# Performance work log

Measured on AMD Instinct MI355X. Metric: run time of the kernel, lower is better.

## Reference

```python
import jax, jax.numpy as jnp
import numpy as np

N, D, K = 262144, 64, 1024


def setup_inputs() -> dict:
    key = jax.random.key(0)
    kx, kc = jax.random.split(key)
    x = jax.random.normal(kx, (N, D), dtype=jnp.float32)
    codebook = jax.random.normal(kc, (K, D), dtype=jnp.float32)
    return {"x": x, "codebook": codebook}


def reference(x, codebook):
    # VQTokenizer.encode: cdist(x, codebook) -> argmin -> gather.
    # squared distances equals argmin over cdist (sqrt is monotone).
    x2 = jnp.sum(x * x, axis=-1, keepdims=True)            # (N, 1)
    c2 = jnp.sum(codebook * codebook, axis=-1)             # (K,)
    d2 = x2 + c2[None, :] - 2.0 * jnp.einsum('nd,kd->nk', x, codebook)  # (N, K)
    encoded = jnp.argmin(d2, axis=1)                       # (N,) int
    quantized = jnp.take(codebook, encoded, axis=0)        # (N, D)
    return encoded, quantized
```

## Files before the change

kernel.cpp:

```cpp
#include <hip/hip_runtime.h>
#include <hip/hip_bf16.h>

#define NPTS 262144
#define DDIM 64
#define KCB  1024
#define CHUNK 64
#define NCHUNK (KCB / CHUNK)
#define GPC (CHUNK / 16)
#define PPB 128

typedef __attribute__((ext_vector_type(8))) short short8;
typedef __attribute__((ext_vector_type(4))) float f32x4;

static __device__ __forceinline__ unsigned short f2bf_rne(float f) {
    union { float f; unsigned u; } v; v.f = f;
    unsigned r = v.u + 0x7FFFu + ((v.u >> 16) & 1u);
    return (unsigned short)(r >> 16);
}
static __device__ __forceinline__ float bf2f(unsigned short h) {
    union { unsigned u; float f; } v; v.u = ((unsigned)h) << 16;
    return v.f;
}
static __device__ __forceinline__ bool beats(float sa, int ka, float sb, int kb) {
    return (sa > sb) || (sa == sb && ka < kb);
}
static __device__ __forceinline__ float keyf(float acc, unsigned inv) {
    return __uint_as_float((__float_as_uint(acc) & 0xFFFFFFC0u) | inv);
}

__global__ __launch_bounds__(256) void c2n_kernel(const float* __restrict__ cb,
                                                  float* __restrict__ c2n) {
    int k = blockIdx.x * blockDim.x + threadIdx.x;
    if (k >= KCB) return;
    const float4* row = (const float4*)(cb + (size_t)k * DDIM);
    float s0 = 0.f, s1 = 0.f, s2 = 0.f, s3 = 0.f;
#pragma unroll
    for (int j = 0; j < DDIM / 4; ++j) {
        float4 a = row[j];
        s0 = __builtin_fmaf(a.x, a.x, s0);
        s1 = __builtin_fmaf(a.y, a.y, s1);
        s2 = __builtin_fmaf(a.z, a.z, s2);
        s3 = __builtin_fmaf(a.w, a.w, s3);
    }
    c2n[k] = 256.0f - 0.5f * ((s0 + s1) + (s2 + s3));
}

__global__ __launch_bounds__(256) void pack_kernel(const float* __restrict__ cb,
                                                   unsigned short* __restrict__ G) {
    int t = blockIdx.x * 256 + threadIdx.x;
    int r = t >> 3, d8 = t & 7;
    const float4* src = (const float4*)(cb + (size_t)r * DDIM + d8 * 8);
    float4 v0 = src[0], v1 = src[1];
    float vv[8] = {v0.x, v0.y, v0.z, v0.w, v1.x, v1.y, v1.z, v1.w};
    short8 h, l;
#pragma unroll
    for (int j = 0; j < 8; ++j) {
        unsigned short hb = f2bf_rne(vv[j]);
        h[j] = (short)hb;
        l[j] = (short)f2bf_rne(vv[j] - bf2f(hb));
    }
    int c = r >> 6, g = (r >> 4) & 3, col = r & 15;
    int ks = d8 >> 2, q = d8 & 3;
    size_t base = (size_t)c * 8192 + g * 1024 + ks * 512 + q * 128 + col * 8;
    *(short8*)(G + base) = h;
    *(short8*)(G + base + 4096) = l;
}

struct BFrag { short8 h0, l0, h1, l1; };

__global__ __launch_bounds__(256, 4) void vq_main(const float* __restrict__ x,
                                                  const float* __restrict__ cb,
                                                  const float* __restrict__ c2n,
                                                  const unsigned short* __restrict__ G,
                                                  float* __restrict__ out) {
    __shared__ unsigned short frag[2][CHUNK * DDIM * 2];
    __shared__ int lds_bk1[PPB];
    __shared__ int lds_bk2[PPB];

    const int tid = threadIdx.x;
    const int lane = tid & 63;
    const int wave = tid >> 6;
    const int b15 = lane & 15;
    const int q = lane >> 4;
    const int blk_base = blockIdx.x * PPB;
    const int wave_base = blk_base + wave * 32;
    const int lane_off = lane * 16;

    short8 Ahi[2][2], Alo[2][2];
#pragma unroll
    for (int t = 0; t < 2; ++t) {
        const float* xr = x + (size_t)(wave_base + t * 16 + b15) * DDIM + q * 8;
#pragma unroll
        for (int ks = 0; ks < 2; ++ks) {
            float4 v0 = *(const float4*)(xr + ks * 32);
            float4 v1 = *(const float4*)(xr + ks * 32 + 4);
            float vv[8] = {v0.x, v0.y, v0.z, v0.w, v1.x, v1.y, v1.z, v1.w};
            short8 h, l;
#pragma unroll
            for (int j = 0; j < 8; ++j) {
                unsigned short hb = f2bf_rne(vv[j]);
                h[j] = (short)hb;
                l[j] = (short)f2bf_rne(vv[j] - bf2f(hb));
            }
            Ahi[t][ks] = h;
            Alo[t][ks] = l;
        }
    }

    float b1[8], b2[8];
#pragma unroll
    for (int i = 0; i < 8; ++i) { b1[i] = 0.0f; b2[i] = 0.0f; }

#define STAGE(cc, buf)                                                                     \
    {                                                                                      \
        const unsigned char* gsrc = (const unsigned char*)G + (size_t)(cc) * 16384 + tid * 16; \
        unsigned char* ldst = (unsigned char*)&frag[buf][0] + tid * 16;                    \
        _Pragma("unroll") for (int it = 0; it < 4; ++it)                                   \
            __builtin_amdgcn_global_load_lds(                                              \
                (const __attribute__((address_space(1))) unsigned int*)(gsrc + it * 4096), \
                (__attribute__((address_space(3))) unsigned int*)(ldst + it * 4096),       \
                16, 0, 0);                                                                 \
    }

    STAGE(0, 0);
    __syncthreads();

    const f32x4 zed = (f32x4){0.f, 0.f, 0.f, 0.f};

    for (int cc = 0; cc < NCHUNK; ++cc) {
        const int cur = cc & 1;
        if (cc + 1 < NCHUNK) STAGE(cc + 1, cur ^ 1);
        const unsigned char* fb = (const unsigned char*)&frag[cur][0];

#pragma unroll
        for (int g = 0; g < GPC; ++g) {
            const int gg = cc * GPC + g;
            const unsigned inv = 63u - (unsigned)gg;
            BFrag B;
            {
                const unsigned char* p_ = fb + (size_t)g * 2048 + lane_off;
                B.h0 = *(const short8*)(p_);
                B.l0 = *(const short8*)(p_ + 8192);
                B.h1 = *(const short8*)(p_ + 1024);
                B.l1 = *(const short8*)(p_ + 9216);
            }
            const float cg = c2n[gg * 16 + b15];
            const f32x4 cvec = (f32x4){cg, cg, cg, cg};

            f32x4 aa[2], ab[2], ac[2];
            __builtin_amdgcn_s_setprio(1);
#pragma unroll
            for (int t = 0; t < 2; ++t) {
                aa[t] = __builtin_amdgcn_mfma_f32_16x16x32_bf16(Ahi[t][0], B.h0, cvec, 0, 0, 0);
                ab[t] = __builtin_amdgcn_mfma_f32_16x16x32_bf16(Ahi[t][0], B.l0, zed, 0, 0, 0);
                ac[t] = __builtin_amdgcn_mfma_f32_16x16x32_bf16(Alo[t][0], B.h0, zed, 0, 0, 0);
                aa[t] = __builtin_amdgcn_mfma_f32_16x16x32_bf16(Ahi[t][1], B.h1, aa[t], 0, 0, 0);
                ab[t] = __builtin_amdgcn_mfma_f32_16x16x32_bf16(Ahi[t][1], B.l1, ab[t], 0, 0, 0);
                ac[t] = __builtin_amdgcn_mfma_f32_16x16x32_bf16(Alo[t][1], B.h1, ac[t], 0, 0, 0);
            }
            __builtin_amdgcn_s_setprio(0);

#pragma unroll
            for (int t = 0; t < 2; ++t) {
                const f32x4 acc = (aa[t] + ab[t]) + ac[t];
#pragma unroll
                for (int r = 0; r < 4; ++r) {
                    const int i = t * 4 + r;
                    const float kk = keyf(acc[r], inv);
                    b2[i] = __builtin_amdgcn_fmed3f(kk, b1[i], b2[i]);
                    b1[i] = fmaxf(b1[i], kk);
                }
            }
        }
        __syncthreads();
    }
#undef STAGE

    unsigned int K1[8], K2[8];
    int I1[8], I2[8];
#pragma unroll
    for (int i = 0; i < 8; ++i) {
        K1[i] = __float_as_uint(b1[i]); I1[i] = (int)(63u - (K1[i] & 63u)) * 16 + b15;
        K2[i] = __float_as_uint(b2[i]); I2[i] = (int)(63u - (K2[i] & 63u)) * 16 + b15;
    }
#pragma unroll
    for (int m = 1; m < 16; m <<= 1) {
#pragma unroll
        for (int i = 0; i < 8; ++i) {
            unsigned int o1 = __shfl_xor(K1[i], m); int oi1 = __shfl_xor(I1[i], m);
            unsigned int o2 = __shfl_xor(K2[i], m); int oi2 = __shfl_xor(I2[i], m);
            bool ob = (o1 > K1[i]) || (o1 == K1[i] && oi1 < I1[i]);
            unsigned int nk1, nk2; int ni1, ni2;
            if (ob) {
                nk1 = o1; ni1 = oi1;
                bool sb = (K1[i] > o2) || (K1[i] == o2 && I1[i] < oi2);
                nk2 = sb ? K1[i] : o2; ni2 = sb ? I1[i] : oi2;
            } else {
                nk1 = K1[i]; ni1 = I1[i];
                bool sb = (o1 > K2[i]) || (o1 == K2[i] && oi1 < I2[i]);
                nk2 = sb ? o1 : K2[i]; ni2 = sb ? oi1 : I2[i];
            }
            K1[i] = nk1; I1[i] = ni1; K2[i] = nk2; I2[i] = ni2;
        }
    }

    if (b15 == 0) {
#pragma unroll
        for (int t = 0; t < 2; ++t)
#pragma unroll
            for (int r = 0; r < 4; ++r) {
                int pl = wave * 32 + t * 16 + q * 4 + r;
                lds_bk1[pl] = I1[t * 4 + r];
                lds_bk2[pl] = I2[t * 4 + r];
            }
    }
    __syncthreads();

    const int pid = tid >> 1;
    const int p = blk_base + pid;
    const int ksel = (tid & 1) ? lds_bk2[pid] : lds_bk1[pid];
    const float4* xr = (const float4*)(x + (size_t)p * DDIM);
    const float4* cr = (const float4*)(cb + (size_t)ksel * DDIM);
    float da = 0.f, db = 0.f;
#pragma unroll
    for (int j = 0; j < 16; ++j) {
        float4 xv = xr[j];
        float4 u = cr[j];
        da = __builtin_fmaf(xv.x, u.x, da); db = __builtin_fmaf(xv.y, u.y, db);
        da = __builtin_fmaf(xv.z, u.z, da); db = __builtin_fmaf(xv.w, u.w, db);
    }
    float a = (da + db) + c2n[ksel];
    float oa = __shfl_xor(a, 1);
    int ok = __shfl_xor(ksel, 1);
    const bool first = ((tid & 1) == 0);
    float a1 = first ? a : oa; int k1 = first ? ksel : ok;
    float a2 = first ? oa : a; int k2 = first ? ok : ksel;
    int kf = beats(a1, k1, a2, k2) ? k1 : k2;

    if (first) out[p] = (float)kf;
    const float4* cf = (const float4*)(cb + (size_t)kf * DDIM + (tid & 1) * 32);
    float4* qo = (float4*)(out + NPTS + (size_t)p * DDIM + (tid & 1) * 32);
#pragma unroll
    for (int j = 0; j < 8; ++j) qo[j] = cf[j];
}

extern "C" void kernel_launch(void* const* d_in, const int* in_sizes, int n_in,
                              void* d_out, int out_size, void* d_ws, size_t ws_size,
                              hipStream_t stream) {
    const float* x = (const float*)d_in[0];
    const float* cb = (const float*)d_in[1];
    float* c2n = (float*)d_ws;
    unsigned short* G = (unsigned short*)((char*)d_ws + 4096);

    hipLaunchKernelGGL(c2n_kernel, dim3(KCB / 256), dim3(256), 0, stream, cb, c2n);
    hipLaunchKernelGGL(pack_kernel, dim3(KCB * 8 / 256), dim3(256), 0, stream, cb, G);
    hipLaunchKernelGGL(vq_main, dim3(NPTS / PPB), dim3(256), 0, stream,
                       x, cb, c2n, G, (float*)d_out);
}
```

Before: 153.7 us.

## Switch to fp16 split-x MFMA with top-3 candidates and exact fp32 rescoring

```diff
diff --git a/kernel.cpp b/kernel.cpp
--- a/kernel.cpp
+++ b/kernel.cpp
@@ -4,23 +4,14 @@
 #define NPTS 262144
 #define DDIM 64
 #define KCB  1024
-#define CHUNK 64
+#define CHUNK 128
 #define NCHUNK (KCB / CHUNK)
 #define GPC (CHUNK / 16)
-#define PPB 128
-
-typedef __attribute__((ext_vector_type(8))) short short8;
+#define PPB 256
+
+typedef __attribute__((ext_vector_type(8))) _Float16 half8;
 typedef __attribute__((ext_vector_type(4))) float f32x4;
 
-static __device__ __forceinline__ unsigned short f2bf_rne(float f) {
-    union { float f; unsigned u; } v; v.f = f;
-    unsigned r = v.u + 0x7FFFu + ((v.u >> 16) & 1u);
-    return (unsigned short)(r >> 16);
-}
-static __device__ __forceinline__ float bf2f(unsigned short h) {
-    union { unsigned u; float f; } v; v.u = ((unsigned)h) << 16;
-    return v.f;
-}
 static __device__ __forceinline__ bool beats(float sa, int ka, float sb, int kb) {
     return (sa > sb) || (sa == sb && ka < kb);
 }
@@ -29,20 +20,25 @@
 }
 
 __global__ __launch_bounds__(256) void c2n_kernel(const float* __restrict__ cb,
-                                                  float* __restrict__ c2n) {
+                                                  float* __restrict__ c2h,
+                                                  float* __restrict__ c2x) {
     int k = blockIdx.x * blockDim.x + threadIdx.x;
     if (k >= KCB) return;
     const float4* row = (const float4*)(cb + (size_t)k * DDIM);
-    float s0 = 0.f, s1 = 0.f, s2 = 0.f, s3 = 0.f;
+    float sh = 0.f, sx = 0.f;
 #pragma unroll
     for (int j = 0; j < DDIM / 4; ++j) {
         float4 a = row[j];
-        s0 = __builtin_fmaf(a.x, a.x, s0);
-        s1 = __builtin_fmaf(a.y, a.y, s1);
-        s2 = __builtin_fmaf(a.z, a.z, s2);
-        s3 = __builtin_fmaf(a.w, a.w, s3);
-    }
-    c2n[k] = 256.0f - 0.5f * ((s0 + s1) + (s2 + s3));
+        float v[4] = {a.x, a.y, a.z, a.w};
+#pragma unroll
+        for (int e = 0; e < 4; ++e) {
+            float h = (float)(_Float16)v[e];
+            sh = __builtin_fmaf(h, h, sh);
+            sx = __builtin_fmaf(v[e], v[e], sx);
+        }
+    }
+    c2h[k] = 256.0f - 0.5f * sh;
+    c2x[k] = 256.0f - 0.5f * sx;
 }
 
 __global__ __launch_bounds__(256) void pack_kernel(const float* __restrict__ cb,
@@ -52,30 +48,26 @@
     const float4* src = (const float4*)(cb + (size_t)r * DDIM + d8 * 8);
     float4 v0 = src[0], v1 = src[1];
     float vv[8] = {v0.x, v0.y, v0.z, v0.w, v1.x, v1.y, v1.z, v1.w};
-    short8 h, l;
-#pragma unroll
-    for (int j = 0; j < 8; ++j) {
-        unsigned short hb = f2bf_rne(vv[j]);
-        h[j] = (short)hb;
-        l[j] = (short)f2bf_rne(vv[j] - bf2f(hb));
-    }
-    int c = r >> 6, g = (r >> 4) & 3, col = r & 15;
+    half8 h;
+#pragma unroll
+    for (int j = 0; j < 8; ++j) h[j] = (_Float16)vv[j];
+    int c = r >> 7, g = (r >> 4) & 7, col = r & 15;
     int ks = d8 >> 2, q = d8 & 3;
     size_t base = (size_t)c * 8192 + g * 1024 + ks * 512 + q * 128 + col * 8;
-    *(short8*)(G + base) = h;
-    *(short8*)(G + base + 4096) = l;
-}
-
-struct BFrag { short8 h0, l0, h1, l1; };
-
-__global__ __launch_bounds__(256, 4) void vq_main(const float* __restrict__ x,
+    *(half8*)(G + base) = h;
+}
+
+__global__ __launch_bounds__(512, 4) void vq_main(const float* __restrict__ x,
                                                   const float* __restrict__ cb,
-                                                  const float* __restrict__ c2n,
+                                                  const float* __restrict__ c2h,
+                                                  const float* __restrict__ c2x,
                                                   const unsigned short* __restrict__ G,
                                                   float* __restrict__ out) {
-    __shared__ unsigned short frag[2][CHUNK * DDIM * 2];
+    __shared__ unsigned short frag[2][CHUNK * DDIM];
+    __shared__ float lds_c2f[KCB];
     __shared__ int lds_bk1[PPB];
     __shared__ int lds_bk2[PPB];
+    __shared__ int lds_bk3[PPB];
 
     const int tid = threadIdx.x;
     const int lane = tid & 63;
@@ -86,7 +78,7 @@
     const int wave_base = blk_base + wave * 32;
     const int lane_off = lane * 16;
 
-    short8 Ahi[2][2], Alo[2][2];
+    half8 Ah[2][2], Al[2][2];
 #pragma unroll
     for (int t = 0; t < 2; ++t) {
         const float* xr = x + (size_t)(wave_base + t * 16 + b15) * DDIM + q * 8;
@@ -95,37 +87,37 @@
             float4 v0 = *(const float4*)(xr + ks * 32);
             float4 v1 = *(const float4*)(xr + ks * 32 + 4);
             float vv[8] = {v0.x, v0.y, v0.z, v0.w, v1.x, v1.y, v1.z, v1.w};
-            short8 h, l;
+            half8 h, l;
 #pragma unroll
             for (int j = 0; j < 8; ++j) {
-                unsigned short hb = f2bf_rne(vv[j]);
-                h[j] = (short)hb;
-                l[j] = (short)f2bf_rne(vv[j] - bf2f(hb));
-            }
-            Ahi[t][ks] = h;
-            Alo[t][ks] = l;
-        }
-    }
-
-    float b1[8], b2[8];
-#pragma unroll
-    for (int i = 0; i < 8; ++i) { b1[i] = 0.0f; b2[i] = 0.0f; }
+                _Float16 hh = (_Float16)vv[j];
+                h[j] = hh;
+                l[j] = (_Float16)(vv[j] - (float)hh);
+            }
+            Ah[t][ks] = h;
+            Al[t][ks] = l;
+        }
+    }
+
+    float b1[8], b2[8], b3[8];
+#pragma unroll
+    for (int i = 0; i < 8; ++i) { b1[i] = 0.0f; b2[i] = 0.0f; b3[i] = 0.0f; }
 
 #define STAGE(cc, buf)                                                                     \
     {                                                                                      \
         const unsigned char* gsrc = (const unsigned char*)G + (size_t)(cc) * 16384 + tid * 16; \
         unsigned char* ldst = (unsigned char*)&frag[buf][0] + tid * 16;                    \
-        _Pragma("unroll") for (int it = 0; it < 4; ++it)                                   \
+        _Pragma("unroll") for (int it = 0; it < 2; ++it)                                   \
             __builtin_amdgcn_global_load_lds(                                              \
-                (const __attribute__((address_space(1))) unsigned int*)(gsrc + it * 4096), \
-                (__attribute__((address_space(3))) unsigned int*)(ldst + it * 4096),       \
+                (const __attribute__((address_space(1))) unsigned int*)(gsrc + it * 8192), \
+                (__attribute__((address_space(3))) unsigned int*)(ldst + it * 8192),       \
                 16, 0, 0);                                                                 \
     }
 
     STAGE(0, 0);
+    lds_c2f[tid] = c2h[tid];
+    lds_c2f[tid + 512] = c2h[tid + 512];
     __syncthreads();
-
-    const f32x4 zed = (f32x4){0.f, 0.f, 0.f, 0.f};
 
     for (int cc = 0; cc < NCHUNK; ++cc) {
         const int cur = cc & 1;
@@ -136,71 +128,70 @@
         for (int g = 0; g < GPC; ++g) {
             const int gg = cc * GPC + g;
             const unsigned inv = 63u - (unsigned)gg;
-            BFrag B;
-            {
-                const unsigned char* p_ = fb + (size_t)g * 2048 + lane_off;
-                B.h0 = *(const short8*)(p_);
-                B.l0 = *(const short8*)(p_ + 8192);
-                B.h1 = *(const short8*)(p_ + 1024);
-                B.l1 = *(const short8*)(p_ + 9216);
-            }
-            const float cg = c2n[gg * 16 + b15];
+            const unsigned char* p_ = fb + (size_t)g * 2048 + lane_off;
+            const half8 B0 = *(const half8*)(p_);
+            const half8 B1 = *(const half8*)(p_ + 1024);
+            const float cg = lds_c2f[gg * 16 + b15];
             const f32x4 cvec = (f32x4){cg, cg, cg, cg};
 
-            f32x4 aa[2], ab[2], ac[2];
+            f32x4 acc[2];
             __builtin_amdgcn_s_setprio(1);
 #pragma unroll
             for (int t = 0; t < 2; ++t) {
-                aa[t] = __builtin_amdgcn_mfma_f32_16x16x32_bf16(Ahi[t][0], B.h0, cvec, 0, 0, 0);
-                ab[t] = __builtin_amdgcn_mfma_f32_16x16x32_bf16(Ahi[t][0], B.l0, zed, 0, 0, 0);
-                ac[t] = __builtin_amdgcn_mfma_f32_16x16x32_bf16(Alo[t][0], B.h0, zed, 0, 0, 0);
-                aa[t] = __builtin_amdgcn_mfma_f32_16x16x32_bf16(Ahi[t][1], B.h1, aa[t], 0, 0, 0);
-                ab[t] = __builtin_amdgcn_mfma_f32_16x16x32_bf16(Ahi[t][1], B.l1, ab[t], 0, 0, 0);
-                ac[t] = __builtin_amdgcn_mfma_f32_16x16x32_bf16(Alo[t][1], B.h1, ac[t], 0, 0, 0);
+                acc[t] = __builtin_amdgcn_mfma_f32_16x16x32_f16(Ah[t][0], B0, cvec, 0, 0, 0);
+                acc[t] = __builtin_amdgcn_mfma_f32_16x16x32_f16(Al[t][0], B0, acc[t], 0, 0, 0);
+                acc[t] = __builtin_amdgcn_mfma_f32_16x16x32_f16(Ah[t][1], B1, acc[t], 0, 0, 0);
+                acc[t] = __builtin_amdgcn_mfma_f32_16x16x32_f16(Al[t][1], B1, acc[t], 0, 0, 0);
             }
             __builtin_amdgcn_s_setprio(0);
 
 #pragma unroll
-            for (int t = 0; t < 2; ++t) {
-                const f32x4 acc = (aa[t] + ab[t]) + ac[t];
+            for (int t = 0; t < 2; ++t)
 #pragma unroll
                 for (int r = 0; r < 4; ++r) {
                     const int i = t * 4 + r;
-                    const float kk = keyf(acc[r], inv);
-                    b2[i] = __builtin_amdgcn_fmed3f(kk, b1[i], b2[i]);
+                    const float kk = keyf(acc[t][r], inv);
+                    const float n3 = __builtin_amdgcn_fmed3f(kk, b2[i], b3[i]);
+                    const float n2 = __builtin_amdgcn_fmed3f(kk, b1[i], b2[i]);
                     b1[i] = fmaxf(b1[i], kk);
+                    b2[i] = n2;
+                    b3[i] = n3;
                 }
-            }
         }
         __syncthreads();
     }
 #undef STAGE
 
-    unsigned int K1[8], K2[8];
-    int I1[8], I2[8];
+    unsigned int K1[8], K2[8], K3[8];
+    int I1[8], I2[8], I3[8];
 #pragma unroll
     for (int i = 0; i < 8; ++i) {
         K1[i] = __float_as_uint(b1[i]); I1[i] = (int)(63u - (K1[i] & 63u)) * 16 + b15;
         K2[i] = __float_as_uint(b2[i]); I2[i] = (int)(63u - (K2[i] & 63u)) * 16 + b15;
+        K3[i] = __float_as_uint(b3[i]); I3[i] = (int)(63u - (K3[i] & 63u)) * 16 + b15;
     }
 #pragma unroll
     for (int m = 1; m < 16; m <<= 1) {
 #pragma unroll
         for (int i = 0; i < 8; ++i) {
-            unsigned int o1 = __shfl_xor(K1[i], m); int oi1 = __shfl_xor(I1[i], m);
-            unsigned int o2 = __shfl_xor(K2[i], m); int oi2 = __shfl_xor(I2[i], m);
-            bool ob = (o1 > K1[i]) || (o1 == K1[i] && oi1 < I1[i]);
-            unsigned int nk1, nk2; int ni1, ni2;
-            if (ob) {
-                nk1 = o1; ni1 = oi1;
-                bool sb = (K1[i] > o2) || (K1[i] == o2 && I1[i] < oi2);
-                nk2 = sb ? K1[i] : o2; ni2 = sb ? I1[i] : oi2;
-            } else {
-                nk1 = K1[i]; ni1 = I1[i];
-                bool sb = (o1 > K2[i]) || (o1 == K2[i] && oi1 < I2[i]);
-                nk2 = sb ? o1 : K2[i]; ni2 = sb ? oi1 : I2[i];
-            }
-            K1[i] = nk1; I1[i] = ni1; K2[i] = nk2; I2[i] = ni2;
+            unsigned int ok[3]; int oi[3];
+            ok[0] = __shfl_xor(K1[i], m); oi[0] = __shfl_xor(I1[i], m);
+            ok[1] = __shfl_xor(K2[i], m); oi[1] = __shfl_xor(I2[i], m);
+            ok[2] = __shfl_xor(K3[i], m); oi[2] = __shfl_xor(I3[i], m);
+#pragma unroll
+            for (int s = 0; s < 3; ++s) {
+                const unsigned int kk = ok[s]; const int ii = oi[s];
+                bool c1 = (kk > K1[i]) || (kk == K1[i] && ii < I1[i]);
+                bool c2 = (kk > K2[i]) || (kk == K2[i] && ii < I2[i]);
+                bool c3 = (kk > K3[i]) || (kk == K3[i] && ii < I3[i]);
+                unsigned int nk3 = c2 ? K2[i] : (c3 ? kk : K3[i]);
+                int ni3 = c2 ? I2[i] : (c3 ? ii : I3[i]);
+                unsigned int nk2 = c1 ? K1[i] : (c2 ? kk : K2[i]);
+                int ni2 = c1 ? I1[i] : (c2 ? ii : I2[i]);
+                unsigned int nk1 = c1 ? kk : K1[i];
+                int ni1 = c1 ? ii : I1[i];
+                K1[i] = nk1; I1[i] = ni1; K2[i] = nk2; I2[i] = ni2; K3[i] = nk3; I3[i] = ni3;
+            }
         }
     }
 
@@ -212,29 +203,42 @@
                 int pl = wave * 32 + t * 16 + q * 4 + r;
                 lds_bk1[pl] = I1[t * 4 + r];
                 lds_bk2[pl] = I2[t * 4 + r];
+                lds_bk3[pl] = I3[t * 4 + r];
             }
     }
     __syncthreads();
 
     const int pid = tid >> 1;
     const int p = blk_base + pid;
-    const int ksel = (tid & 1) ? lds_bk2[pid] : lds_bk1[pid];
+    const bool first = ((tid & 1) == 0);
+    const int ka = first ? lds_bk1[pid] : lds_bk2[pid];
+    const int kb = lds_bk3[pid];
     const float4* xr = (const float4*)(x + (size_t)p * DDIM);
-    const float4* cr = (const float4*)(cb + (size_t)ksel * DDIM);
-    float da = 0.f, db = 0.f;
+    const float4* ca = (const float4*)(cb + (size_t)ka * DDIM);
+    const float4* cbp = (const float4*)(cb + (size_t)kb * DDIM);
+    float daa = 0.f, dab = 0.f, dba = 0.f, dbb = 0.f;
 #pragma unroll
     for (int j = 0; j < 16; ++j) {
         float4 xv = xr[j];
-        float4 u = cr[j];
-        da = __builtin_fmaf(xv.x, u.x, da); db = __builtin_fmaf(xv.y, u.y, db);
-        da = __builtin_fmaf(xv.z, u.z, da); db = __builtin_fmaf(xv.w, u.w, db);
-    }
-    float a = (da + db) + c2n[ksel];
-    float oa = __shfl_xor(a, 1);
-    int ok = __shfl_xor(ksel, 1);
-    const bool first = ((tid & 1) == 0);
-    float a1 = first ? a : oa; int k1 = first ? ksel : ok;
-    float a2 = first ? oa : a; int k2 = first ? ok : ksel;
+        float4 u = ca[j];
+        daa = __builtin_fmaf(xv.x, u.x, daa); dab = __builtin_fmaf(xv.y, u.y, dab);
+        daa = __builtin_fmaf(xv.z, u.z, daa); dab = __builtin_fmaf(xv.w, u.w, dab);
+        if (!first) {
+            float4 w = cbp[j];
+            dba = __builtin_fmaf(xv.x, w.x, dba); dbb = __builtin_fmaf(xv.y, w.y, dbb);
+            dba = __builtin_fmaf(xv.z, w.z, dba); dbb = __builtin_fmaf(xv.w, w.w, dbb);
+        }
+    }
+    float aa = (daa + dab) + c2x[ka];
+    int kaa = ka;
+    if (!first) {
+        float ab = (dba + dbb) + c2x[kb];
+        if (beats(ab, kb, aa, kaa)) { aa = ab; kaa = kb; }
+    }
+    float oa = __shfl_xor(aa, 1);
+    int okk = __shfl_xor(kaa, 1);
+    float a1 = first ? aa : oa; int k1 = first ? kaa : okk;
+    float a2 = first ? oa : aa; int k2 = first ? okk : kaa;
     int kf = beats(a1, k1, a2, k2) ? k1 : k2;
 
     if (first) out[p] = (float)kf;
@@ -249,11 +253,12 @@
                               hipStream_t stream) {
     const float* x = (const float*)d_in[0];
     const float* cb = (const float*)d_in[1];
-    float* c2n = (float*)d_ws;
-    unsigned short* G = (unsigned short*)((char*)d_ws + 4096);
-
-    hipLaunchKernelGGL(c2n_kernel, dim3(KCB / 256), dim3(256), 0, stream, cb, c2n);
+    float* c2h = (float*)d_ws;
+    float* c2x = (float*)((char*)d_ws + 4096);
+    unsigned short* G = (unsigned short*)((char*)d_ws + 8192);
+
+    hipLaunchKernelGGL(c2n_kernel, dim3(KCB / 256), dim3(256), 0, stream, cb, c2h, c2x);
     hipLaunchKernelGGL(pack_kernel, dim3(KCB * 8 / 256), dim3(256), 0, stream, cb, G);
-    hipLaunchKernelGGL(vq_main, dim3(NPTS / PPB), dim3(256), 0, stream,
-                       x, cb, c2n, G, (float*)d_out);
-}
+    hipLaunchKernelGGL(vq_main, dim3(NPTS / PPB), dim3(512), 0, stream,
+                       x, cb, c2h, c2x, G, (float*)d_out);
+}
```

Result: slower. 167.5 us (+9.0%).
